# Kernel optimization log

Measured on AMD Instinct MI355X. Metric: run time of the kernel, lower is better.

Reference implementation:

```python
import math
import jax, jax.numpy as jnp
import numpy as np

NUM_HEADS = 32
NUM_KV_HEADS = 8
HEAD_SIZE = 128
FEATURE_DIM = 64
SEQ_LEN = 2048
WINDOW_SIZE = 64
EPS = 1e-12
MASK_VALUE = -100000000.0


def _make_masks(n: int, w: int):
    # block-diagonal ones(w,w) tiles, plus the rolled (sub-diagonal) tiles
    m = math.ceil(n / w)
    mask = np.kron(np.eye(m), np.ones((w, w)))
    mask = mask + np.roll(mask, -w, axis=-1)
    mask = mask[:n, :n]
    mask_window = np.tril(mask).astype(bool)[None, None]          # [1,1,n,n]
    mask_linear = np.tril(1.0 - mask).astype(bool)[None, None]    # [1,1,n,n]
    return jnp.asarray(mask_window), jnp.asarray(mask_linear)


def _feature_map(w, x):
    # f(x) = clamp(cat(softmax(xW), softmax(-xW)), min=eps)
    z = jnp.einsum('hdf,bhld->bhlf', w, x)
    return jnp.clip(
        jnp.concatenate([jax.nn.softmax(z, axis=-1), jax.nn.softmax(-z, axis=-1)], axis=-1),
        EPS, None)


def setup_inputs() -> dict:
    key = jax.random.key(0)
    ks = jax.random.split(key, 6)
    return {
        'query': jax.random.normal(ks[0], (SEQ_LEN, NUM_HEADS * HEAD_SIZE), dtype=jnp.float32),
        'key': jax.random.normal(ks[1], (SEQ_LEN, NUM_KV_HEADS * HEAD_SIZE), dtype=jnp.float32),
        'value': jax.random.normal(ks[2], (SEQ_LEN, NUM_KV_HEADS * HEAD_SIZE), dtype=jnp.float32),
        'fmap_q_w': 0.02 * jax.random.normal(ks[3], (NUM_HEADS, HEAD_SIZE, FEATURE_DIM), dtype=jnp.float32),
        'fmap_k_w': 0.02 * jax.random.normal(ks[4], (NUM_HEADS, HEAD_SIZE, FEATURE_DIM), dtype=jnp.float32),
        'window_factors': jax.random.normal(ks[5], (1, NUM_HEADS, 1, 1), dtype=jnp.float32),
    }


def reference(query, key, value, fmap_q_w, fmap_k_w, window_factors):
    T = query.shape[0]
    q = query.reshape(T, NUM_HEADS, HEAD_SIZE)
    k = key.reshape(T, NUM_KV_HEADS, HEAD_SIZE)
    v = value.reshape(T, NUM_KV_HEADS, HEAD_SIZE)
    rep = NUM_HEADS // NUM_KV_HEADS
    k = jnp.repeat(k, rep, axis=1)
    v = jnp.repeat(v, rep, axis=1)
    # [T,H,D] -> [1,H,T,D]
    q = jnp.moveaxis(q, 0, -2)[None]
    k = jnp.moveaxis(k, 0, -2)[None]
    v = jnp.moveaxis(v, 0, -2)[None]

    f_q = _feature_map(fmap_q_w, q)  # [1,H,T,2F]
    f_k = _feature_map(fmap_k_w, k)
    wf = jax.nn.sigmoid(window_factors)

    mask_window, mask_linear = _make_masks(SEQ_LEN, WINDOW_SIZE)
    mask_window = mask_window[:, :, :T, :T]
    mask_linear = mask_linear[:, :, :T, :T]

    # sliding-window softmax term
    a_sm = jnp.einsum('bhmd,bhnd->bhmn', q, k) * (HEAD_SIZE ** -0.5)
    a_sm = jnp.where(mask_window, a_sm, MASK_VALUE)
    a_sm_max = jnp.max(a_sm, axis=-1, keepdims=True)
    a_sm = wf * jnp.exp(a_sm - a_sm_max)
    sum_sm = jnp.sum(a_sm, axis=-1, keepdims=True)

    # linear feature-map term (linear_factor = 1)
    a_ln = jnp.einsum('bhmd,bhnd->bhmn', f_q, f_k)
    a_ln = jnp.where(mask_linear, a_ln, 0.0)
    sum_ln = jnp.sum(a_ln, axis=-1, keepdims=True)

    y = jnp.einsum('bhmn,bhnd->bhmd', a_sm + a_ln, v)
    return y / (sum_sm + sum_ln)
```

## Files before the change

kernel.cpp:

```cpp
#include <hip/hip_runtime.h>
#include <math.h>

#define T_SEQ 2048
#define NH    32
#define NKV   8
#define HS    128
#define FD    64
#define NBLK  32
#define EPSF  1e-12f
#define LDP   136

typedef unsigned short u16;
typedef __bf16 bf16x8 __attribute__((ext_vector_type(8)));
typedef float  f32x4  __attribute__((ext_vector_type(4)));

__device__ __forceinline__ u16 f2b(float f) {
  unsigned u = __builtin_bit_cast(unsigned, f);
  return (u16)((u + 0x7fffu + ((u >> 16) & 1u)) >> 16);
}

#define FQB_OFF 0
#define FKT_OFF 16777216
#define ST_OFF  33554432
#define VT_OFF  71303168
#define WT_OFF  75497472

__global__ __launch_bounds__(256) void k_pre(
    const float* __restrict__ wq, const float* __restrict__ wk,
    const float* __restrict__ vg,
    u16* __restrict__ WT, u16* __restrict__ VT)
{
  __shared__ float sB[128 * 68];
  const int bx = blockIdx.x, tid = threadIdx.x;

  if (bx < 64) {
    const int h = bx >> 1, isk = bx & 1;
    const float* src = (isk ? wk : wq) + (size_t)h * HS * FD;
    for (int idx = tid * 4; idx < 8192; idx += 1024) {
      int r = idx >> 6, c = idx & 63;
      *(float4*)(sB + r * 68 + c) = *(const float4*)(src + idx);
    }
    __syncthreads();
    u16* dst = WT + ((size_t)(isk * NH + h)) * 8192;
    for (int i = 0; i < 8; ++i) {
      int ch = tid + i * 256;
      int f = ch >> 5, d4 = (ch & 31) * 4;
      ushort4 u;
      u.x = f2b(sB[(d4 + 0) * 68 + f]);
      u.y = f2b(sB[(d4 + 1) * 68 + f]);
      u.z = f2b(sB[(d4 + 2) * 68 + f]);
      u.w = f2b(sB[(d4 + 3) * 68 + f]);
      *(ushort4*)(dst + f * 128 + d4) = u;
    }
  } else {
    const int idx2 = bx - 64;
    const int b = idx2 & 31, kvh = idx2 >> 5;
    float* sV = sB;
    for (int idx = tid * 4; idx < 8192; idx += 1024) {
      int r = idx >> 7, c = idx & 127;
      *(float4*)(sV + r * 129 + c) = *(const float4*)(vg + (size_t)(b * 64 + r) * (NKV * HS) + kvh * HS + c);
    }
    __syncthreads();
    const int lane = tid & 63, w = tid >> 6;
#pragma unroll
    for (int i = 0; i < 32; ++i) {
      int d = w * 32 + i;
      VT[((size_t)(kvh * 128 + d)) * T_SEQ + b * 64 + lane] = f2b(sV[lane * 129 + d]);
    }
  }
}

__global__ __launch_bounds__(256) void k_fmap(
    const float* __restrict__ qg, const float* __restrict__ kg,
    const u16* __restrict__ WT,
    u16* __restrict__ fqb, u16* __restrict__ FKT)
{
  __shared__ __align__(16) u16 smem[2 * 64 * 136];
  u16* sX = smem;
  u16* sW = smem + 64 * 136;
  const int lt = blockIdx.x, h = blockIdx.y, isk = blockIdx.z;
  const int tid = threadIdx.x, lane = tid & 63, w = tid >> 6;
  const int quad = lane >> 4, txn = lane & 15;

  const float* xbase = isk ? (kg + (h >> 2) * HS) : (qg + h * HS);
  const int    xstr  = isk ? (NKV * HS) : (NH * HS);
  for (int idx = tid * 4; idx < 8192; idx += 1024) {
    int r = idx >> 7, c = idx & 127;
    float4 v4 = *(const float4*)(xbase + (size_t)(lt * 64 + r) * xstr + c);
    ushort4 u; u.x = f2b(v4.x); u.y = f2b(v4.y); u.z = f2b(v4.z); u.w = f2b(v4.w);
    *(ushort4*)(sX + r * 136 + c) = u;
  }
  const u16* wt = WT + ((size_t)(isk * NH + h)) * 8192;
  for (int i = 0; i < 4; ++i) {
    int ch = tid + i * 256;
    int row = ch >> 4, d8 = (ch & 15) * 8;
    *(uint4*)(sW + row * 136 + d8) = *(const uint4*)(wt + row * 128 + d8);
  }
  __syncthreads();

  const int arow = w * 16 + txn;
  const f32x4 vzero = {0.f, 0.f, 0.f, 0.f};
  f32x4 zt[4] = {vzero, vzero, vzero, vzero};
#pragma unroll
  for (int ks = 0; ks < 4; ++ks) {
    bf16x8 a = *(const bf16x8*)(sX + arow * 136 + ks * 32 + quad * 8);
#pragma unroll
    for (int nt = 0; nt < 4; ++nt) {
      bf16x8 bb = *(const bf16x8*)(sW + (nt * 16 + txn) * 136 + ks * 32 + quad * 8);
      zt[nt] = __builtin_amdgcn_mfma_f32_16x16x32_bf16(a, bb, zt[nt], 0, 0, 0);
    }
  }

  float E1[4][4], E2[4][4];
#pragma unroll
  for (int r = 0; r < 4; ++r) {
    float zv[4];
    float mx = -1e30f, mn = 1e30f;
#pragma unroll
    for (int nt = 0; nt < 4; ++nt) {
      zv[nt] = zt[nt][r];
      mx = fmaxf(mx, zv[nt]); mn = fminf(mn, zv[nt]);
    }
#pragma unroll
    for (int o = 1; o < 16; o <<= 1) {
      mx = fmaxf(mx, __shfl_xor(mx, o));
      mn = fminf(mn, __shfl_xor(mn, o));
    }
    float e1[4], e2[4], s1 = 0.f, s2 = 0.f;
#pragma unroll
    for (int nt = 0; nt < 4; ++nt) {
      e1[nt] = __expf(zv[nt] - mx); s1 += e1[nt];
      e2[nt] = __expf(mn - zv[nt]); s2 += e2[nt];
    }
#pragma unroll
    for (int o = 1; o < 16; o <<= 1) { s1 += __shfl_xor(s1, o); s2 += __shfl_xor(s2, o); }
    float r1 = 1.f / s1, r2 = 1.f / s2;
#pragma unroll
    for (int nt = 0; nt < 4; ++nt) {
      E1[r][nt] = fmaxf(e1[nt] * r1, EPSF);
      E2[r][nt] = fmaxf(e2[nt] * r2, EPSF);
    }
  }

  __syncthreads();

  if (!isk) {
#pragma unroll
    for (int r = 0; r < 4; ++r) {
      int row = w * 16 + quad * 4 + r;
#pragma unroll
      for (int nt = 0; nt < 4; ++nt) {
        sX[row * 136 + nt * 16 + txn]      = f2b(E1[r][nt]);
        sX[row * 136 + 64 + nt * 16 + txn] = f2b(E2[r][nt]);
      }
    }
    __syncthreads();
    u16* ob = fqb + ((size_t)(h * NBLK + lt)) * 8192;
    for (int i = 0; i < 4; ++i) {
      int ch = tid + i * 256;
      int row = ch >> 4, f8 = (ch & 15) * 8;
      *(uint4*)(ob + row * 128 + f8) = *(const uint4*)(sX + row * 136 + f8);
    }
  } else {
#pragma unroll
    for (int r = 0; r < 4; ++r) {
      int j = w * 16 + quad * 4 + r;
#pragma unroll
      for (int nt = 0; nt < 4; ++nt) {
        sX[(nt * 16 + txn) * 68 + j]        = f2b(E1[r][nt]);
        sX[(nt * 16 + txn + 64) * 68 + j]   = f2b(E2[r][nt]);
      }
    }
    __syncthreads();
    u16* ob = FKT + (size_t)h * 128 * T_SEQ + lt * 64;
    for (int i = 0; i < 8; ++i) {
      int ch = tid + i * 256;
      int row = ch >> 4, j4 = (ch & 15) * 4;
      *(ushort4*)(ob + (size_t)row * T_SEQ + j4) = *(const ushort4*)(sX + row * 68 + j4);
    }
  }
}

__global__ __launch_bounds__(256) void k_scan(
    const u16* __restrict__ FKT, const u16* __restrict__ VT, u16* __restrict__ ST)
{
  __shared__ __align__(16) u16 sVT[16 * 72];
  __shared__ __align__(16) u16 sFK[64 * 72];
  __shared__ __align__(16) u16 sOne[16 * 72];
  __shared__ __align__(16) u16 sO[16 * 72];
  const int dc = blockIdx.x, fh = blockIdx.y, h = blockIdx.z;
  const int tid = threadIdx.x, lane = tid & 63, w = tid >> 6;
  const int quad = lane >> 4, txn = lane & 15;
  const bool doz = (dc == 0);

  for (int idx = tid * 8; idx < 16 * 72; idx += 2048) {
    ushort4 o4; o4.x = 0x3F80; o4.y = 0x3F80; o4.z = 0x3F80; o4.w = 0x3F80;
    *(ushort4*)(sOne + idx) = o4;
    *(ushort4*)(sOne + idx + 4) = o4;
  }

  const u16* vbase = VT + ((size_t)((h >> 2) * 128 + dc * 16)) * T_SEQ;
  const u16* fbase = FKT + ((size_t)(h * 128 + fh * 64)) * T_SEQ;

  const int srow = tid >> 4, sj4 = (tid & 15) * 4;
  ushort4 rv, rf[4];
  rv = *(const ushort4*)(vbase + (size_t)srow * T_SEQ + sj4);
#pragma unroll
  for (int i = 0; i < 4; ++i) {
    int ch = tid + i * 256;
    int fr = ch >> 4, fj4 = (ch & 15) * 4;
    rf[i] = *(const ushort4*)(fbase + (size_t)fr * T_SEQ + fj4);
  }

  const f32x4 vzero = {0.f, 0.f, 0.f, 0.f};
  f32x4 acc = vzero, zacc = vzero;

  for (int b = 0; b < NBLK; ++b) {
    __syncthreads();
    *(ushort4*)(sVT + srow * 72 + sj4) = rv;
#pragma unroll
    for (int i = 0; i < 4; ++i) {
      int ch = tid + i * 256;
      int fr = ch >> 4, fj4 = (ch & 15) * 4;
      *(ushort4*)(sFK + fr * 72 + fj4) = rf[i];
    }
    __syncthreads();
    if (b + 1 < NBLK) {
      rv = *(const ushort4*)(vbase + (size_t)srow * T_SEQ + (b + 1) * 64 + sj4);
#pragma unroll
      for (int i = 0; i < 4; ++i) {
        int ch = tid + i * 256;
        int fr = ch >> 4, fj4 = (ch & 15) * 4;
        rf[i] = *(const ushort4*)(fbase + (size_t)fr * T_SEQ + (b + 1) * 64 + fj4);
      }
    }
#pragma unroll
    for (int ks = 0; ks < 2; ++ks) {
      bf16x8 a  = *(const bf16x8*)(sVT + txn * 72 + ks * 32 + quad * 8);
      bf16x8 bb = *(const bf16x8*)(sFK + (w * 16 + txn) * 72 + ks * 32 + quad * 8);
      acc = __builtin_amdgcn_mfma_f32_16x16x32_bf16(a, bb, acc, 0, 0, 0);
      if (doz) {
        bf16x8 ao = *(const bf16x8*)(sOne + txn * 72 + ks * 32 + quad * 8);
        zacc = __builtin_amdgcn_mfma_f32_16x16x32_bf16(ao, bb, zacc, 0, 0, 0);
      }
    }
#pragma unroll
    for (int r = 0; r < 4; ++r)
      sO[(quad * 4 + r) * 72 + w * 16 + txn] = f2b(acc[r]);
    if (doz && quad == 0)
      ST[(((size_t)(h * NBLK + b)) * 144 + 128) * 128 + fh * 64 + w * 16 + txn] = f2b(zacc[0]);
    __syncthreads();
    *(ushort4*)(ST + (((size_t)(h * NBLK + b)) * 144 + dc * 16 + srow) * 128 + fh * 64 + sj4)
        = *(const ushort4*)(sO + srow * 72 + sj4);
  }
}

__global__ __launch_bounds__(256, 4) void k_main(
    const float* __restrict__ qg, const float* __restrict__ kg,
    const u16* __restrict__ fqb, const u16* __restrict__ ST, const u16* __restrict__ VT,
    const float* __restrict__ wfac, float* __restrict__ out)
{
  __shared__ __align__(16) u16 RA[64 * LDP];
  __shared__ __align__(16) u16 RB[64 * LDP];
  __shared__ __align__(16) u16 sz[128];
  const int B = blockIdx.x, h = blockIdx.y, tid = threadIdx.x;
  const int lane = tid & 63, w = tid >> 6;
  const int quad = lane >> 4, txn = lane & 15;
  const int arow = w * 16 + txn;
  const int koff = quad * 8;

  const f32x4 vzero = {0.f, 0.f, 0.f, 0.f};
  f32x4 y[8];
#pragma unroll
  for (int t = 0; t < 8; ++t) y[t] = vzero;
  float sln[4] = {0.f, 0.f, 0.f, 0.f};
  const bf16x8 bzero = {0, 0, 0, 0, 0, 0, 0, 0};

  if (B >= 2) {
    const u16* fsrc = fqb + ((size_t)(h * NBLK + B)) * 8192;
    for (int idx = tid * 4; idx < 8192; idx += 1024) {
      int r = idx >> 7, c = idx & 127;
      *(ushort4*)(RA + r * LDP + c) = *(const ushort4*)(fsrc + idx);
    }
    const u16* ssrc = ST + ((size_t)(h * NBLK + (B - 2))) * 18432;
    for (int idx = tid * 4; idx < 8192; idx += 1024) {
      int r = idx >> 7, c = idx & 127;
      *(ushort4*)(RB + r * LDP + c) = *(const ushort4*)(ssrc + idx);
    }
    if (tid < 32) *(ushort4*)(sz + tid * 4) = *(const ushort4*)(ssrc + 16384 + tid * 4);
    __syncthreads();
    f32x4 yz = vzero;
#pragma unroll
    for (int ks = 0; ks < 4; ++ks) {
      bf16x8 a = *(const bf16x8*)(RA + arow * LDP + ks * 32 + koff);
#pragma unroll
      for (int t = 0; t < 4; ++t) {
        bf16x8 bb = *(const bf16x8*)(RB + (t * 16 + txn) * LDP + ks * 32 + koff);
        y[t] = __builtin_amdgcn_mfma_f32_16x16x32_bf16(a, bb, y[t], 0, 0, 0);
      }
      bf16x8 bz = (txn == 0) ? *(const bf16x8*)(sz + ks * 32 + koff) : bzero;
      yz = __builtin_amdgcn_mfma_f32_16x16x32_bf16(a, bz, yz, 0, 0, 0);
    }
    __syncthreads();
    for (int idx = tid * 4; idx < 8192; idx += 1024) {
      int r = idx >> 7, c = idx & 127;
      *(ushort4*)(RB + r * LDP + c) = *(const ushort4*)(ssrc + 8192 + idx);
    }
    __syncthreads();
#pragma unroll
    for (int ks = 0; ks < 4; ++ks) {
      bf16x8 a = *(const bf16x8*)(RA + arow * LDP + ks * 32 + koff);
#pragma unroll
      for (int t = 4; t < 8; ++t) {
        bf16x8 bb = *(const bf16x8*)(RB + (t * 16 + txn - 64) * LDP + ks * 32 + koff);
        y[t] = __builtin_amdgcn_mfma_f32_16x16x32_bf16(a, bb, y[t], 0, 0, 0);
      }
    }
#pragma unroll
    for (int r = 0; r < 4; ++r) sln[r] = __shfl(yz[r], lane & 48);
    __syncthreads();
  }

  const int kb0 = (B >= 1) ? B - 1 : 0;
  {
    const float* qs = qg + (size_t)(B * 64) * (NH * HS) + h * HS;
    for (int idx = tid * 4; idx < 8192; idx += 1024) {
      int r = idx >> 7, c = idx & 127;
      float4 v4 = *(const float4*)(qs + (size_t)r * (NH * HS) + c);
      ushort4 u; u.x = f2b(v4.x); u.y = f2b(v4.y); u.z = f2b(v4.z); u.w = f2b(v4.w);
      *(ushort4*)(RA + r * LDP + c) = u;
    }
    const float* kd = kg + (size_t)(B * 64) * (NKV * HS) + (h >> 2) * HS;
    for (int idx = tid * 4; idx < 8192; idx += 1024) {
      int r = idx >> 7, c = idx & 127;
      float4 v4 = *(const float4*)(kd + (size_t)r * (NKV * HS) + c);
      ushort4 u; u.x = f2b(v4.x); u.y = f2b(v4.y); u.z = f2b(v4.z); u.w = f2b(v4.w);
      *(ushort4*)(RB + r * LDP + c) = u;
    }
  }
  __syncthreads();

  f32x4 s[8];
#pragma unroll
  for (int t = 0; t < 8; ++t) s[t] = vzero;
#pragma unroll
  for (int ks = 0; ks < 4; ++ks) {
    bf16x8 a = *(const bf16x8*)(RA + arow * LDP + ks * 32 + koff);
#pragma unroll
    for (int t = 0; t < 4; ++t) {
      bf16x8 bb = *(const bf16x8*)(RB + (t * 16 + txn) * LDP + ks * 32 + koff);
      s[4 + t] = __builtin_amdgcn_mfma_f32_16x16x32_bf16(a, bb, s[4 + t], 0, 0, 0);
    }
  }

  if (B >= 1) {
    __syncthreads();
    const float* kd = kg + (size_t)(kb0 * 64) * (NKV * HS) + (h >> 2) * HS;
    for (int idx = tid * 4; idx < 8192; idx += 1024) {
      int r = idx >> 7, c = idx & 127;
      float4 v4 = *(const float4*)(kd + (size_t)r * (NKV * HS) + c);
      ushort4 u; u.x = f2b(v4.x); u.y = f2b(v4.y); u.z = f2b(v4.z); u.w = f2b(v4.w);
      *(ushort4*)(RB + r * LDP + c) = u;
    }
    __syncthreads();
#pragma unroll
    for (int ks = 0; ks < 4; ++ks) {
      bf16x8 a = *(const bf16x8*)(RA + arow * LDP + ks * 32 + koff);
#pragma unroll
      for (int t = 0; t < 4; ++t) {
        bf16x8 bb = *(const bf16x8*)(RB + (t * 16 + txn) * LDP + ks * 32 + koff);
        s[t] = __builtin_amdgcn_mfma_f32_16x16x32_bf16(a, bb, s[t], 0, 0, 0);
      }
    }
  }

  float wf = wfac[h];
  wf = 1.f / (1.f + __expf(-wf));
  const float scale = 0.08838834764831845f;
  float ssum[4];
#pragma unroll
  for (int r = 0; r < 4; ++r) {
    const int irow = w * 16 + quad * 4 + r;
    float sv[8];
    float m = -1e30f;
#pragma unroll
    for (int t = 0; t < 8; ++t) {
      float x = s[t][r] * scale;
      bool msk = (t < 4) ? (B == 0) : ((t - 4) * 16 + txn > irow);
      x = msk ? -1e30f : x;
      sv[t] = x;
      m = fmaxf(m, x);
    }
#pragma unroll
    for (int o = 1; o < 16; o <<= 1) m = fmaxf(m, __shfl_xor(m, o));
    float ss = 0.f;
#pragma unroll
    for (int t = 0; t < 8; ++t) {
      float e = (sv[t] > -1e29f) ? wf * __expf(sv[t] - m) : 0.f;
      ss += e;
      RA[irow * LDP + t * 16 + txn] = f2b(e);
    }
#pragma unroll
    for (int o = 1; o < 16; o <<= 1) ss += __shfl_xor(ss, o);
    ssum[r] = ss;
  }
  __syncthreads();

  const u16* vts = VT + (size_t)((h >> 2) * 128) * T_SEQ;
  for (int idx = tid * 4; idx < 8192; idx += 1024) {
    int r = idx >> 7, c = idx & 127;
    int key = (c < 64) ? (kb0 * 64 + c) : (B * 64 + (c - 64));
    *(ushort4*)(RB + r * LDP + c) = *(const ushort4*)(vts + (size_t)r * T_SEQ + key);
  }
  __syncthreads();
#pragma unroll
  for (int ks = 0; ks < 4; ++ks) {
    if (B == 0 && ks < 2) continue;
    bf16x8 a = *(const bf16x8*)(RA + arow * LDP + ks * 32 + koff);
#pragma unroll
    for (int t = 0; t < 4; ++t) {
      bf16x8 bb = *(const bf16x8*)(RB + (t * 16 + txn) * LDP + ks * 32 + koff);
      y[t] = __builtin_amdgcn_mfma_f32_16x16x32_bf16(a, bb, y[t], 0, 0, 0);
    }
  }
  __syncthreads();

  for (int idx = tid * 4; idx < 8192; idx += 1024) {
    int r = idx >> 7, c = idx & 127;
    int key = (c < 64) ? (kb0 * 64 + c) : (B * 64 + (c - 64));
    *(ushort4*)(RB + r * LDP + c) = *(const ushort4*)(vts + (size_t)(r + 64) * T_SEQ + key);
  }
  __syncthreads();
#pragma unroll
  for (int ks = 0; ks < 4; ++ks) {
    if (B == 0 && ks < 2) continue;
    bf16x8 a = *(const bf16x8*)(RA + arow * LDP + ks * 32 + koff);
#pragma unroll
    for (int t = 4; t < 8; ++t) {
      bf16x8 bb = *(const bf16x8*)(RB + (t * 16 + txn - 64) * LDP + ks * 32 + koff);
      y[t] = __builtin_amdgcn_mfma_f32_16x16x32_bf16(a, bb, y[t], 0, 0, 0);
    }
  }

  const size_t obase = ((size_t)h * T_SEQ + B * 64) * HS;
#pragma unroll
  for (int r = 0; r < 4; ++r) {
    float inv = 1.f / (ssum[r] + sln[r]);
    int irow = w * 16 + quad * 4 + r;
#pragma unroll
    for (int t = 0; t < 8; ++t)
      out[obase + (size_t)irow * HS + t * 16 + txn] = y[t][r] * inv;
  }
}

extern "C" void kernel_launch(void* const* d_in, const int* in_sizes, int n_in,
                              void* d_out, int out_size, void* d_ws, size_t ws_size,
                              hipStream_t stream) {
  const float* q    = (const float*)d_in[0];
  const float* k    = (const float*)d_in[1];
  const float* v    = (const float*)d_in[2];
  const float* wq   = (const float*)d_in[3];
  const float* wk   = (const float*)d_in[4];
  const float* wfac = (const float*)d_in[5];
  float* out = (float*)d_out;
  char* wsb = (char*)d_ws;

  u16* fqb = (u16*)(wsb + FQB_OFF);
  u16* FKT = (u16*)(wsb + FKT_OFF);
  u16* ST  = (u16*)(wsb + ST_OFF);
  u16* VT  = (u16*)(wsb + VT_OFF);
  u16* WT  = (u16*)(wsb + WT_OFF);

  k_pre  <<<dim3(320),         256, 0, stream>>>(wq, wk, v, WT, VT);
  k_fmap <<<dim3(NBLK, NH, 2), 256, 0, stream>>>(q, k, WT, fqb, FKT);
  k_scan <<<dim3(8, 2, NH),    256, 0, stream>>>(FKT, VT, ST);
  k_main <<<dim3(NBLK, NH),    256, 0, stream>>>(q, k, fqb, ST, VT, wfac, out);
}
```

Measured before the change: 176.9 us.

## Register-prefetch next tiles in k_main and drop LDS staging in k_scan

k_main now issues the global loads for the next operand tile (ST second half, Q/K fp32, previous K block, both V halves) into registers before the current MFMA phase, then stores them to LDS afterwards. Memory latency overlaps with compute instead of being exposed between barriers, and the loads are widened to 16-byte vectors. k_scan replaces the LDS ones-matrix with a register constant and writes its accumulators straight to global memory, removing one LDS buffer and a barrier per block. The cost is many more live registers under launch_bounds(256,4), which risks spills, and k_scan's direct stores are less coalesced.

```diff
diff --git a/kernel.cpp b/kernel.cpp
--- a/kernel.cpp
+++ b/kernel.cpp
@@ -24,6 +24,42 @@
 #define ST_OFF  33554432
 #define VT_OFF  71303168
 #define WT_OFF  75497472
+
+__device__ __forceinline__ void ldg_bf(uint4 r[4], const u16* __restrict__ src, int tid) {
+#pragma unroll
+  for (int i = 0; i < 4; ++i) r[i] = *(const uint4*)(src + tid * 8 + i * 2048);
+}
+__device__ __forceinline__ void sts_bf(u16* buf, const uint4 r[4], int tid) {
+#pragma unroll
+  for (int i = 0; i < 4; ++i) {
+    int idx = tid * 8 + i * 2048, rr = idx >> 7, c = idx & 127;
+    *(uint4*)(buf + rr * LDP + c) = r[i];
+  }
+}
+__device__ __forceinline__ void ldg_f32(float4 r[8], const float* __restrict__ base, int stride, int tid) {
+#pragma unroll
+  for (int i = 0; i < 8; ++i) {
+    int idx = tid * 4 + i * 1024, rr = idx >> 7, c = idx & 127;
+    r[i] = *(const float4*)(base + (size_t)rr * stride + c);
+  }
+}
+__device__ __forceinline__ void sts_f32(u16* buf, const float4 r[8], int tid) {
+#pragma unroll
+  for (int i = 0; i < 8; ++i) {
+    int idx = tid * 4 + i * 1024, rr = idx >> 7, c = idx & 127;
+    ushort4 u; u.x = f2b(r[i].x); u.y = f2b(r[i].y); u.z = f2b(r[i].z); u.w = f2b(r[i].w);
+    *(ushort4*)(buf + rr * LDP + c) = u;
+  }
+}
+__device__ __forceinline__ void ldg_vt(uint4 r[4], const u16* __restrict__ vts,
+                                       int rofs, int kb0, int B, int tid) {
+#pragma unroll
+  for (int i = 0; i < 4; ++i) {
+    int idx = tid * 8 + i * 2048, rr = (idx >> 7) + rofs, c = idx & 127;
+    int key = (c < 64) ? (kb0 * 64 + c) : (B * 64 + (c - 64));
+    r[i] = *(const uint4*)(vts + (size_t)rr * T_SEQ + key);
+  }
+}
 
 __global__ __launch_bounds__(256) void k_pre(
     const float* __restrict__ wq, const float* __restrict__ wk,
@@ -186,18 +222,14 @@
 {
   __shared__ __align__(16) u16 sVT[16 * 72];
   __shared__ __align__(16) u16 sFK[64 * 72];
-  __shared__ __align__(16) u16 sOne[16 * 72];
-  __shared__ __align__(16) u16 sO[16 * 72];
   const int dc = blockIdx.x, fh = blockIdx.y, h = blockIdx.z;
   const int tid = threadIdx.x, lane = tid & 63, w = tid >> 6;
   const int quad = lane >> 4, txn = lane & 15;
   const bool doz = (dc == 0);
 
-  for (int idx = tid * 8; idx < 16 * 72; idx += 2048) {
-    ushort4 o4; o4.x = 0x3F80; o4.y = 0x3F80; o4.z = 0x3F80; o4.w = 0x3F80;
-    *(ushort4*)(sOne + idx) = o4;
-    *(ushort4*)(sOne + idx + 4) = o4;
-  }
+  bf16x8 vone;
+#pragma unroll
+  for (int j = 0; j < 8; ++j) vone[j] = (__bf16)1.0f;
 
   const u16* vbase = VT + ((size_t)((h >> 2) * 128 + dc * 16)) * T_SEQ;
   const u16* fbase = FKT + ((size_t)(h * 128 + fh * 64)) * T_SEQ;
@@ -239,19 +271,14 @@
       bf16x8 a  = *(const bf16x8*)(sVT + txn * 72 + ks * 32 + quad * 8);
       bf16x8 bb = *(const bf16x8*)(sFK + (w * 16 + txn) * 72 + ks * 32 + quad * 8);
       acc = __builtin_amdgcn_mfma_f32_16x16x32_bf16(a, bb, acc, 0, 0, 0);
-      if (doz) {
-        bf16x8 ao = *(const bf16x8*)(sOne + txn * 72 + ks * 32 + quad * 8);
-        zacc = __builtin_amdgcn_mfma_f32_16x16x32_bf16(ao, bb, zacc, 0, 0, 0);
-      }
-    }
+      if (doz) zacc = __builtin_amdgcn_mfma_f32_16x16x32_bf16(vone, bb, zacc, 0, 0, 0);
+    }
+    u16* Sb = ST + (((size_t)(h * NBLK + b)) * 144 + dc * 16) * 128 + fh * 64;
 #pragma unroll
     for (int r = 0; r < 4; ++r)
-      sO[(quad * 4 + r) * 72 + w * 16 + txn] = f2b(acc[r]);
+      Sb[(quad * 4 + r) * 128 + w * 16 + txn] = f2b(acc[r]);
     if (doz && quad == 0)
       ST[(((size_t)(h * NBLK + b)) * 144 + 128) * 128 + fh * 64 + w * 16 + txn] = f2b(zacc[0]);
-    __syncthreads();
-    *(ushort4*)(ST + (((size_t)(h * NBLK + b)) * 144 + dc * 16 + srow) * 128 + fh * 64 + sj4)
-        = *(const ushort4*)(sO + srow * 72 + sj4);
   }
 }
 
@@ -276,18 +303,26 @@
   float sln[4] = {0.f, 0.f, 0.f, 0.f};
   const bf16x8 bzero = {0, 0, 0, 0, 0, 0, 0, 0};
 
+  const int kb0 = (B >= 1) ? B - 1 : 0;
+  const float* qs  = qg + (size_t)(B * 64) * (NH * HS) + h * HS;
+  const float* kdB = kg + (size_t)(B * 64) * (NKV * HS) + (h >> 2) * HS;
+  const float* kdP = kg + (size_t)(kb0 * 64) * (NKV * HS) + (h >> 2) * HS;
+  const u16*   vts = VT + (size_t)((h >> 2) * 128) * T_SEQ;
+
+  uint4  pA[4], pB[4];
+  float4 qf[8], kf[8];
+
   if (B >= 2) {
     const u16* fsrc = fqb + ((size_t)(h * NBLK + B)) * 8192;
-    for (int idx = tid * 4; idx < 8192; idx += 1024) {
-      int r = idx >> 7, c = idx & 127;
-      *(ushort4*)(RA + r * LDP + c) = *(const ushort4*)(fsrc + idx);
-    }
     const u16* ssrc = ST + ((size_t)(h * NBLK + (B - 2))) * 18432;
-    for (int idx = tid * 4; idx < 8192; idx += 1024) {
-      int r = idx >> 7, c = idx & 127;
-      *(ushort4*)(RB + r * LDP + c) = *(const ushort4*)(ssrc + idx);
-    }
-    if (tid < 32) *(ushort4*)(sz + tid * 4) = *(const ushort4*)(ssrc + 16384 + tid * 4);
+    ldg_bf(pA, fsrc, tid);
+    ldg_bf(pB, ssrc, tid);
+    ushort4 zr;
+    if (tid < 32) zr = *(const ushort4*)(ssrc + 16384 + tid * 4);
+    sts_bf(RA, pA, tid);
+    sts_bf(RB, pB, tid);
+    if (tid < 32) *(ushort4*)(sz + tid * 4) = zr;
+    ldg_bf(pB, ssrc + 8192, tid);
     __syncthreads();
     f32x4 yz = vzero;
 #pragma unroll
@@ -302,10 +337,9 @@
       yz = __builtin_amdgcn_mfma_f32_16x16x32_bf16(a, bz, yz, 0, 0, 0);
     }
     __syncthreads();
-    for (int idx = tid * 4; idx < 8192; idx += 1024) {
-      int r = idx >> 7, c = idx & 127;
-      *(ushort4*)(RB + r * LDP + c) = *(const ushort4*)(ssrc + 8192 + idx);
-    }
+    sts_bf(RB, pB, tid);
+    ldg_f32(qf, qs, NH * HS, tid);
+    ldg_f32(kf, kdB, NKV * HS, tid);
     __syncthreads();
 #pragma unroll
     for (int ks = 0; ks < 4; ++ks) {
@@ -319,25 +353,14 @@
 #pragma unroll
     for (int r = 0; r < 4; ++r) sln[r] = __shfl(yz[r], lane & 48);
     __syncthreads();
-  }
-
-  const int kb0 = (B >= 1) ? B - 1 : 0;
-  {
-    const float* qs = qg + (size_t)(B * 64) * (NH * HS) + h * HS;
-    for (int idx = tid * 4; idx < 8192; idx += 1024) {
-      int r = idx >> 7, c = idx & 127;
-      float4 v4 = *(const float4*)(qs + (size_t)r * (NH * HS) + c);
-      ushort4 u; u.x = f2b(v4.x); u.y = f2b(v4.y); u.z = f2b(v4.z); u.w = f2b(v4.w);
-      *(ushort4*)(RA + r * LDP + c) = u;
-    }
-    const float* kd = kg + (size_t)(B * 64) * (NKV * HS) + (h >> 2) * HS;
-    for (int idx = tid * 4; idx < 8192; idx += 1024) {
-      int r = idx >> 7, c = idx & 127;
-      float4 v4 = *(const float4*)(kd + (size_t)r * (NKV * HS) + c);
-      ushort4 u; u.x = f2b(v4.x); u.y = f2b(v4.y); u.z = f2b(v4.z); u.w = f2b(v4.w);
-      *(ushort4*)(RB + r * LDP + c) = u;
-    }
-  }
+  } else {
+    ldg_f32(qf, qs, NH * HS, tid);
+    ldg_f32(kf, kdB, NKV * HS, tid);
+  }
+
+  sts_f32(RA, qf, tid);
+  sts_f32(RB, kf, tid);
+  if (B >= 1) ldg_f32(kf, kdP, NKV * HS, tid);
   __syncthreads();
 
   f32x4 s[8];
@@ -355,13 +378,8 @@
 
   if (B >= 1) {
     __syncthreads();
-    const float* kd = kg + (size_t)(kb0 * 64) * (NKV * HS) + (h >> 2) * HS;
-    for (int idx = tid * 4; idx < 8192; idx += 1024) {
-      int r = idx >> 7, c = idx & 127;
-      float4 v4 = *(const float4*)(kd + (size_t)r * (NKV * HS) + c);
-      ushort4 u; u.x = f2b(v4.x); u.y = f2b(v4.y); u.z = f2b(v4.z); u.w = f2b(v4.w);
-      *(ushort4*)(RB + r * LDP + c) = u;
-    }
+    sts_f32(RB, kf, tid);
+    ldg_vt(pB, vts, 0, kb0, B, tid);
     __syncthreads();
 #pragma unroll
     for (int ks = 0; ks < 4; ++ks) {
@@ -372,6 +390,8 @@
         s[t] = __builtin_amdgcn_mfma_f32_16x16x32_bf16(a, bb, s[t], 0, 0, 0);
       }
     }
+  } else {
+    ldg_vt(pB, vts, 0, kb0, B, tid);
   }
 
   float wf = wfac[h];
@@ -406,12 +426,8 @@
   }
   __syncthreads();
 
-  const u16* vts = VT + (size_t)((h >> 2) * 128) * T_SEQ;
-  for (int idx = tid * 4; idx < 8192; idx += 1024) {
-    int r = idx >> 7, c = idx & 127;
-    int key = (c < 64) ? (kb0 * 64 + c) : (B * 64 + (c - 64));
-    *(ushort4*)(RB + r * LDP + c) = *(const ushort4*)(vts + (size_t)r * T_SEQ + key);
-  }
+  sts_bf(RB, pB, tid);
+  ldg_vt(pA, vts, 64, kb0, B, tid);
   __syncthreads();
 #pragma unroll
   for (int ks = 0; ks < 4; ++ks) {
@@ -425,11 +441,7 @@
   }
   __syncthreads();
 
-  for (int idx = tid * 4; idx < 8192; idx += 1024) {
-    int r = idx >> 7, c = idx & 127;
-    int key = (c < 64) ? (kb0 * 64 + c) : (B * 64 + (c - 64));
-    *(ushort4*)(RB + r * LDP + c) = *(const ushort4*)(vts + (size_t)(r + 64) * T_SEQ + key);
-  }
+  sts_bf(RB, pA, tid);
   __syncthreads();
 #pragma unroll
   for (int ks = 0; ks < 4; ++ks) {
```

After: 192.2 us. 8.6% more time.
